# Kernel tuning notes

Hardware: AMD Instinct MI355X
Metric: run time of the kernel (lower is better)

Reference implementation:

```python
import jax, jax.numpy as jnp
import numpy as np

EPS = 1e-7
POS_THR = 0.5   # max_iou assigner positive threshold
NEG_THR = 0.4   # max_iou assigner negative threshold
ALPHA, GAMMA = 0.25, 2.0  # focal loss defaults


def _rand_boxes(key, shape):
    k1, k2 = jax.random.split(key)
    c = jax.random.uniform(k1, shape + (2,), minval=0.05, maxval=0.95)
    wh = jax.random.uniform(k2, shape + (2,), minval=0.02, maxval=0.3)
    return jnp.concatenate([jnp.clip(c - wh / 2, 0, 1), jnp.clip(c + wh / 2, 0, 1)], -1)


def _grid_anchors():
    # 3 anchor sizes per cell on 80x80, 40x40, 20x20 grids -> 25200 anchors, normalized coords
    boxes = []
    for g, sizes in [(80, (0.04, 0.08, 0.12)), (40, (0.1, 0.2, 0.3)), (20, (0.25, 0.45, 0.65))]:
        c = (np.arange(g, dtype=np.float32) + 0.5) / g
        cx, cy = np.meshgrid(c, c)
        for s in sizes:
            boxes.append(np.stack([cx - s / 2, cy - s / 2, cx + s / 2, cy + s / 2], -1).reshape(-1, 4))
    return jnp.asarray(np.concatenate(boxes, 0), dtype=jnp.float32)


def setup_inputs() -> dict:
    key = jax.random.key(0)
    ks = jax.random.split(key, 6)
    N, P, A, C = 32, 100, 25200, 80
    labels = jax.random.randint(ks[0], (N, P), 0, C)
    y_true = jax.nn.one_hot(labels, C, dtype=jnp.float32)
    bbox_true = _rand_boxes(ks[1], (N, P))
    valid = (jnp.arange(P)[None, :] < 30).astype(jnp.float32)  # 30 real boxes, rest zero-padded
    bbox_true = bbox_true * valid[..., None]
    conf_pred = jax.random.uniform(ks[2], (N, A, 1), minval=0.01, maxval=0.99)
    logit_pred = jax.random.uniform(ks[3], (N, A, C), minval=0.01, maxval=0.99)
    bbox_pred = _rand_boxes(ks[4], (N, A))
    anchors = _grid_anchors()
    return {"y_true": y_true, "bbox_true": bbox_true, "conf_pred": conf_pred,
            "logit_pred": logit_pred, "bbox_pred": bbox_pred, "anchors": anchors}


def pairwise_iou(a, b):
    # a: (A,4), b: (P,4) -> (A,P)
    iw = jnp.clip(jnp.minimum(a[:, None, 2], b[None, :, 2]) - jnp.maximum(a[:, None, 0], b[None, :, 0]), 0)
    ih = jnp.clip(jnp.minimum(a[:, None, 3], b[None, :, 3]) - jnp.maximum(a[:, None, 1], b[None, :, 1]), 0)
    inter = iw * ih
    area_a = (a[:, 2] - a[:, 0]) * (a[:, 3] - a[:, 1])
    area_b = (b[:, 2] - b[:, 0]) * (b[:, 3] - b[:, 1])
    return inter / (area_a[:, None] + area_b[None, :] - inter + EPS)


def target_single(y_true, bbox_true, anchors):
    # mask-based equivalent of the dynamic tf.where/gather/scatter target construction
    P = bbox_true.shape[0]
    valid = jnp.any(bbox_true > 0, axis=-1)  # (P,)
    iou = jnp.where(valid[None, :], pairwise_iou(anchors, bbox_true), -1.0)  # (A,P)
    max_iou = iou.max(-1)
    true_idx = iou.argmax(-1)
    pos = max_iou >= POS_THR
    neg = max_iou < NEG_THR
    # low-quality match: best anchor for each valid gt is positive
    gt_max = iou.max(0)
    gt_best = iou.argmax(0)
    lowq = valid & (gt_max > 0)
    pos = pos.astype(jnp.int32).at[gt_best].max(lowq.astype(jnp.int32)).astype(bool)
    true_idx = true_idx.at[gt_best].set(jnp.where(lowq, jnp.arange(P), true_idx[gt_best]))
    neg = neg & ~pos
    state = jnp.where(pos, 1, jnp.where(neg, -1, 0)).astype(jnp.int8)
    C = y_true.shape[-1]
    background = jnp.zeros((C,), jnp.float32).at[0].set(1.0)  # tf.pad(ones,[0,C-1]) default
    tgt_label = jnp.where(pos[:, None], y_true[true_idx], background[None, :])
    tgt_bbox = jnp.where(pos[:, None], bbox_true[true_idx], 0.0)
    return state[:, None], tgt_label, tgt_bbox


def ciou_loss(bt, bp):
    ix1 = jnp.maximum(bt[..., 0], bp[..., 0]); iy1 = jnp.maximum(bt[..., 1], bp[..., 1])
    ix2 = jnp.minimum(bt[..., 2], bp[..., 2]); iy2 = jnp.minimum(bt[..., 3], bp[..., 3])
    inter = jnp.clip(ix2 - ix1, 0) * jnp.clip(iy2 - iy1, 0)
    wt, ht = bt[..., 2] - bt[..., 0], bt[..., 3] - bt[..., 1]
    wp, hp = bp[..., 2] - bp[..., 0], bp[..., 3] - bp[..., 1]
    union = wt * ht + wp * hp - inter + EPS
    iou = inter / union
    cw = jnp.maximum(bt[..., 2], bp[..., 2]) - jnp.minimum(bt[..., 0], bp[..., 0])
    ch = jnp.maximum(bt[..., 3], bp[..., 3]) - jnp.minimum(bt[..., 1], bp[..., 1])
    c2 = cw * cw + ch * ch + EPS
    rho2 = ((bt[..., 0] + bt[..., 2] - bp[..., 0] - bp[..., 2]) ** 2 +
            (bt[..., 1] + bt[..., 3] - bp[..., 1] - bp[..., 3]) ** 2) / 4.0
    v = (4.0 / (np.pi ** 2)) * (jnp.arctan(wt / (ht + EPS)) - jnp.arctan(wp / (hp + EPS))) ** 2
    alpha = jax.lax.stop_gradient(v / (1.0 - iou + v + EPS))
    return 1.0 - iou + rho2 / c2 + alpha * v


def reference(y_true, bbox_true, conf_pred, logit_pred, bbox_pred, anchors):
    state, t_label, t_bbox = jax.vmap(target_single, in_axes=(0, 0, None))(y_true, bbox_true, anchors)
    dtype = logit_pred.dtype
    pw = (state == 1).astype(dtype)   # positive_weight (N,A,1)
    tw = (state != 0).astype(dtype)   # target_weight   (N,A,1)
    avg_factor = jnp.sum(jnp.maximum(jnp.sum(pw, axis=-2), 1.0))
    # score loss: BCE(positive_weight, conf_pred), weighted by target_weight
    p = jnp.clip(conf_pred, EPS, 1.0 - EPS)
    score_l = -(pw * jnp.log(p) + (1.0 - pw) * jnp.log(1.0 - p))
    score_l = jnp.sum(score_l * tw) / avg_factor
    # class loss: focal BCE, weighted by positive_weight
    q = jnp.clip(logit_pred, EPS, 1.0 - EPS)
    pt = t_label * q + (1.0 - t_label) * (1.0 - q)
    at = t_label * ALPHA + (1.0 - t_label) * (1.0 - ALPHA)
    cls_l = -at * (1.0 - pt) ** GAMMA * jnp.log(pt)
    cls_l = jnp.sum(cls_l * pw) / avg_factor
    # bbox loss: CIoU, weighted by positive_weight
    bl = ciou_loss(t_bbox, bbox_pred)[..., None]
    bbox_l = jnp.sum(bl * pw) / avg_factor
    guard = lambda x: jnp.where(jnp.isnan(x) | jnp.isinf(x), jnp.zeros_like(x), x)  # missing_value=0
    return guard(score_l), guard(cls_l), guard(bbox_l)
```

## Files before the change

kernel.cpp:

```cpp
#include <hip/hip_runtime.h>
#include <math.h>

#define EPSF 1e-7f
#define GCHUNK 10
#define NSEG 16

__device__ __forceinline__ int compact_valid(const float4* __restrict__ bt_n, int P, int tid,
                                             float4* scb, int* sidx, float* sarea, int* wcnt) {
    float4 b = make_float4(0.f, 0.f, 0.f, 0.f);
    bool v = false;
    if (tid < P) {
        b = bt_n[tid];
        v = (b.x > 0.f || b.y > 0.f || b.z > 0.f || b.w > 0.f);
    }
    unsigned long long m = __ballot(v);
    int lane = tid & 63, wv = tid >> 6;
    if (lane == 0) wcnt[wv] = __popcll(m);
    int posn = __popcll(m & ((1ull << lane) - 1ull));
    __syncthreads();
    int base = 0;
    for (int w = 0; w < wv; w++) base += wcnt[w];
    int V = wcnt[0] + wcnt[1] + wcnt[2] + wcnt[3];
    if (v) {
        scb[base + posn] = b;
        sidx[base + posn] = tid;
        sarea[base + posn] = (b.z - b.x) * (b.w - b.y);
    }
    __syncthreads();
    return V;
}

__global__ __launch_bounds__(256) void k_gt_all(const float4* __restrict__ bbox_true,
                                                const float4* __restrict__ anchors,
                                                float* __restrict__ pn, float* __restrict__ pd,
                                                int* __restrict__ pi,
                                                unsigned int* __restrict__ done,
                                                int N, int P, int A) {
    __shared__ float4 scb[256];
    __shared__ int    sidx[256];
    __shared__ float  sarea[256];
    __shared__ int    wcnt[4];
    __shared__ float  mn[4][GCHUNK], md[4][GCHUNK];
    __shared__ int    mi[4][GCHUNK];

    int n = blockIdx.y, seg = blockIdx.x, tid = threadIdx.x;
    if (seg == 0 && n == 0 && tid == 0) *done = 0u;
    int lane = tid & 63, wv = tid >> 6;
    int V = compact_valid(bbox_true + (size_t)n * P, P, tid, scb, sidx, sarea, wcnt);
    int len = (A + NSEG - 1) / NSEG;
    int a0 = seg * len;
    int a1 = a0 + len < A ? a0 + len : A;

    for (int c0 = 0; c0 < V; c0 += GCHUNK) {
        int G = V - c0 < GCHUNK ? V - c0 : GCHUNK;
        float bn[GCHUNK], bd[GCHUNK];
        int   bi[GCHUNK];
#pragma unroll
        for (int g = 0; g < GCHUNK; g++) { bn[g] = -1.f; bd[g] = 1.f; bi[g] = 0x7fffffff; }
        for (int a = a0 + tid; a < a1; a += 256) {
            float4 an = anchors[a];
            float aa = (an.z - an.x) * (an.w - an.y);
#pragma unroll
            for (int g = 0; g < GCHUNK; g++) {
                if (g < G) {
                    float4 b = scb[c0 + g];
                    float iw = fminf(an.z, b.z) - fmaxf(an.x, b.x); iw = iw > 0.f ? iw : 0.f;
                    float ih = fminf(an.w, b.w) - fmaxf(an.y, b.y); ih = ih > 0.f ? ih : 0.f;
                    float inter = iw * ih;
                    float den = aa + sarea[c0 + g] - inter + EPSF;
                    if (inter * bd[g] > bn[g] * den) { bn[g] = inter; bd[g] = den; bi[g] = a; }
                }
            }
        }
        for (int off = 32; off > 0; off >>= 1) {
#pragma unroll
            for (int g = 0; g < GCHUNK; g++) {
                float on = __shfl_xor(bn[g], off, 64);
                float od = __shfl_xor(bd[g], off, 64);
                int   oi = __shfl_xor(bi[g], off, 64);
                float l = on * bd[g], r = bn[g] * od;
                if (l > r || (l == r && oi < bi[g])) { bn[g] = on; bd[g] = od; bi[g] = oi; }
            }
        }
        if (lane == 0) {
#pragma unroll
            for (int g = 0; g < GCHUNK; g++) { mn[wv][g] = bn[g]; md[wv][g] = bd[g]; mi[wv][g] = bi[g]; }
        }
        __syncthreads();
        if (tid < G) {
            float Bn = -1.f, Bd = 1.f; int Bi = 0x7fffffff;
            for (int w = 0; w < 4; w++) {
                float cn = mn[w][tid], cd = md[w][tid];
                int ci = mi[w][tid];
                float l = cn * Bd, r = Bn * cd;
                if (l > r || (l == r && ci < Bi)) { Bn = cn; Bd = cd; Bi = ci; }
            }
            int p = sidx[c0 + tid];
            size_t o = ((size_t)n * P + p) * NSEG + seg;
            pn[o] = Bn; pd[o] = Bd; pi[o] = Bi;
        }
        __syncthreads();
    }
}

__global__ __launch_bounds__(128) void k_scatter2(const float4* __restrict__ bbox_true,
                                                  const float* __restrict__ pn,
                                                  const float* __restrict__ pd,
                                                  const int* __restrict__ pi,
                                                  int* __restrict__ ovr_cnt,
                                                  int2* __restrict__ ovr_list,
                                                  int N, int P, int A) {
    int n = blockIdx.x, p = threadIdx.x;
    __shared__ int gb[128];
    __shared__ unsigned char lqs[128];
    __shared__ int cnt;
    if (p == 0) cnt = 0;
    if (p < P) {
        float4 b = bbox_true[(size_t)n * P + p];
        bool valid = (b.x > 0.f || b.y > 0.f || b.z > 0.f || b.w > 0.f);
        int g = 0; bool lq = false;
        if (valid) {
            float Bn = -1.f, Bd = 1.f; int Bi = 0x7fffffff;
            const float* qn = pn + ((size_t)n * P + p) * NSEG;
            const float* qd = pd + ((size_t)n * P + p) * NSEG;
            const int*   qi = pi + ((size_t)n * P + p) * NSEG;
            for (int s = 0; s < NSEG; s++) {
                float cn = qn[s], cd = qd[s]; int ci = qi[s];
                if (cn >= 0.f) {
                    float l = cn * Bd, r = Bn * cd;
                    if (l > r || (l == r && ci < Bi)) { Bn = cn; Bd = cd; Bi = ci; }
                }
            }
            g = Bi;
            lq = (Bn > 0.f);
        }
        gb[p] = g; lqs[p] = lq ? 1 : 0;
    }
    __syncthreads();
    if (p < P) {
        int myidx = gb[p];
        bool anylq = false, islast = true;
        for (int q = 0; q < P; q++) {
            if (gb[q] == myidx) {
                if (lqs[q]) anylq = true;
                if (q > p) islast = false;
            }
        }
        if (islast && anylq) {
            int s = atomicAdd(&cnt, 1);
            ovr_list[(size_t)n * P + s] = make_int2(myidx, lqs[p] ? p : -2);
        }
    }
    __syncthreads();
    if (p == 0) ovr_cnt[n] = cnt;
}

__global__ __launch_bounds__(256) void k_fused(const float4* __restrict__ bbox_true,
                                               const float4* __restrict__ anchors,
                                               const float* __restrict__ conf,
                                               const float* __restrict__ logit,
                                               const float4* __restrict__ bbox_pred,
                                               const float* __restrict__ y_true,
                                               const int* __restrict__ ovr_cnt,
                                               const int2* __restrict__ ovr_list,
                                               double* __restrict__ partial,
                                               unsigned int* __restrict__ done,
                                               float* __restrict__ out,
                                               int N, int P, int A, int C, int BX) {
    int tid = threadIdx.x;
    int n = blockIdx.y;
    int a = blockIdx.x * blockDim.x + tid;
    int lane = tid & 63, wv = tid >> 6;

    __shared__ float4 scb[256];
    __shared__ int    sidx[256];
    __shared__ float  sarea[256];
    __shared__ int    wcnt[4];
    __shared__ int    sflag[256];
    __shared__ int    plist[256];
    __shared__ int    pw4[4];

    sflag[tid] = -1;
    int V = compact_valid(bbox_true + (size_t)n * P, P, tid, scb, sidx, sarea, wcnt);
    int cnt = ovr_cnt[n];
    if (tid < cnt) {
        int2 e = ovr_list[(size_t)n * P + tid];
        int local = e.x - blockIdx.x * 256;
        if (local >= 0 && local < 256) sflag[local] = e.y;
    }
    __syncthreads();

    double sc = 0.0, cl = 0.0, bb = 0.0, pc = 0.0;
    bool pos = false;
    int t = 0;
    if (a < A) {
        float4 an = anchors[a];
        float aa = (an.z - an.x) * (an.w - an.y);
        float bn = -1.f, bd = 1.f; int bi = 0;
        for (int k = 0; k < V; k++) {
            float4 b = scb[k];
            float iw = fminf(an.z, b.z) - fmaxf(an.x, b.x); iw = iw > 0.f ? iw : 0.f;
            float ih = fminf(an.w, b.w) - fmaxf(an.y, b.y); ih = ih > 0.f ? ih : 0.f;
            float inter = iw * ih;
            float den = aa + sarea[k] - inter + EPSF;
            if (inter * bd > bn * den) { bn = inter; bd = den; bi = sidx[k]; }
        }
        bool neg;
        if (V > 0) { pos = (bn >= 0.5f * bd); neg = (bn < 0.4f * bd); }
        else       { pos = false; neg = true; }
        int ov = sflag[tid];
        pos = pos || (ov != -1);
        neg = neg && !pos;
        t = (ov >= 0) ? ov : bi;

        size_t o = (size_t)n * A + a;
        float p = conf[o];
        p = fminf(fmaxf(p, EPSF), 1.f - EPSF);
        if (pos || neg) sc = (double)(-logf(pos ? p : 1.f - p));
        if (pos) {
            pc = 1.0;
            float4 bt = bbox_true[(size_t)n * P + t];
            float4 bp = bbox_pred[o];
            float ix1 = fmaxf(bt.x, bp.x), iy1 = fmaxf(bt.y, bp.y);
            float ix2 = fminf(bt.z, bp.z), iy2 = fminf(bt.w, bp.w);
            float iw = ix2 - ix1; iw = iw > 0.f ? iw : 0.f;
            float ih = iy2 - iy1; ih = ih > 0.f ? ih : 0.f;
            float inter = iw * ih;
            float wt = bt.z - bt.x, ht = bt.w - bt.y;
            float wp = bp.z - bp.x, hp = bp.w - bp.y;
            float uni = wt * ht + wp * hp - inter + EPSF;
            float iou = inter / uni;
            float cw = fmaxf(bt.z, bp.z) - fminf(bt.x, bp.x);
            float ch = fmaxf(bt.w, bp.w) - fminf(bt.y, bp.y);
            float c2 = cw * cw + ch * ch + EPSF;
            float dx = bt.x + bt.z - bp.x - bp.z;
            float dy = bt.y + bt.w - bp.y - bp.w;
            float rho2 = (dx * dx + dy * dy) * 0.25f;
            float dd = atanf(wt / (ht + EPSF)) - atanf(wp / (hp + EPSF));
            float vv = 0.40528473456935109f * dd * dd;
            float al = vv / (1.f - iou + vv + EPSF);
            bb = (double)(1.f - iou + rho2 / c2 + al * vv);
        }
    }

    {
        unsigned long long m = __ballot(pos);
        if (lane == 0) pw4[wv] = __popcll(m);
        int posn = __popcll(m & ((1ull << lane) - 1ull));
        __syncthreads();
        int base = 0;
        for (int w = 0; w < wv; w++) base += pw4[w];
        int npos = pw4[0] + pw4[1] + pw4[2] + pw4[3];
        if (pos) plist[base + posn] = tid | (t << 8);
        __syncthreads();

        for (int i = wv; i < npos; i += 4) {
            int e = plist[i];
            int la = e & 255, tt = e >> 8;
            size_t o = (size_t)n * A + (size_t)blockIdx.x * 256 + la;
            const float* lg = logit + o * C;
            const float* yt = y_true + ((size_t)n * P + tt) * C;
            float s = 0.f;
            for (int c = lane; c < C; c += 64) {
                float tl = yt[c];
                float q = fminf(fmaxf(lg[c], EPSF), 1.f - EPSF);
                float pt = tl * q + (1.f - tl) * (1.f - q);
                float at = tl * 0.25f + (1.f - tl) * 0.75f;
                float om = 1.f - pt;
                s += -at * om * om * logf(pt);
            }
            for (int off = 32; off > 0; off >>= 1) s += __shfl_down(s, off, 64);
            if (lane == 0) cl += (double)s;
        }
    }

    for (int off = 32; off > 0; off >>= 1) {
        sc += __shfl_down(sc, off, 64);
        cl += __shfl_down(cl, off, 64);
        bb += __shfl_down(bb, off, 64);
        pc += __shfl_down(pc, off, 64);
    }
    __shared__ double sred[4][4];
    if (lane == 0) { sred[wv][0] = sc; sred[wv][1] = cl; sred[wv][2] = bb; sred[wv][3] = pc; }
    __syncthreads();
    __shared__ int amLast;
    if (tid == 0) {
        double r0 = 0, r1 = 0, r2 = 0, r3 = 0;
        for (int w = 0; w < 4; w++) {
            r0 += sred[w][0]; r1 += sred[w][1]; r2 += sred[w][2]; r3 += sred[w][3];
        }
        double* row = partial + ((size_t)n * BX + blockIdx.x) * 4;
        row[0] = r0; row[1] = r1; row[2] = r2; row[3] = r3;
        __threadfence();
        unsigned int old = atomicAdd(done, 1u);
        amLast = (old == (unsigned int)(N * BX) - 1u) ? 1 : 0;
    }
    __syncthreads();
    if (!amLast) return;
    __threadfence();

    __shared__ double sh[256];
    __shared__ double res[3];
    __shared__ double shn[64];
    double s0 = 0, s1 = 0, s2 = 0;
    int total = N * BX;
    for (int i = tid; i < total; i += 256) {
        const double* r = partial + (size_t)i * 4;
        s0 += r[0]; s1 += r[1]; s2 += r[2];
    }
    double vals[3] = {s0, s1, s2};
    for (int k = 0; k < 3; k++) {
        sh[tid] = vals[k];
        __syncthreads();
        for (int s = 128; s > 0; s >>= 1) {
            if (tid < s) sh[tid] += sh[tid + s];
            __syncthreads();
        }
        if (tid == 0) res[k] = sh[0];
        __syncthreads();
    }
    int chunks = 256 / N;
    double pcs = 0;
    int nn = tid / chunks, cc = tid % chunks;
    if (nn < N) {
        int per = (BX + chunks - 1) / chunks;
        int j0 = cc * per, j1 = (j0 + per < BX) ? j0 + per : BX;
        for (int j = j0; j < j1; j++) pcs += partial[((size_t)nn * BX + j) * 4 + 3];
    }
    sh[tid] = pcs;
    __syncthreads();
    if (tid < N) {
        double s = 0;
        for (int c2 = 0; c2 < chunks; c2++) s += sh[tid * chunks + c2];
        shn[tid] = s > 1.0 ? s : 1.0;
    }
    __syncthreads();
    if (tid == 0) {
        double avg = 0;
        for (int i = 0; i < N; i++) avg += shn[i];
        for (int k = 0; k < 3; k++) {
            double x = res[k] / avg;
            if (isnan(x) || isinf(x)) x = 0.0;
            out[k] = (float)x;
        }
    }
}

extern "C" void kernel_launch(void* const* d_in, const int* in_sizes, int n_in,
                              void* d_out, int out_size, void* d_ws, size_t ws_size,
                              hipStream_t stream) {
    const float* y_true    = (const float*)d_in[0];
    const float* bbox_true = (const float*)d_in[1];
    const float* conf      = (const float*)d_in[2];
    const float* logit     = (const float*)d_in[3];
    const float* bboxp     = (const float*)d_in[4];
    const float* anchors   = (const float*)d_in[5];

    int A = in_sizes[5] / 4;
    int N = in_sizes[2] / A;
    int P = in_sizes[1] / (4 * N);
    int C = in_sizes[0] / (N * P);

    int BX = (A + 255) / 256;

    char* w = (char*)d_ws;
    auto alloc = [&](size_t bytes) -> void* {
        void* r = (void*)w;
        w += (bytes + 15) & ~(size_t)15;
        return r;
    };
    float*  pn      = (float*)alloc(sizeof(float) * (size_t)N * P * NSEG);
    float*  pd      = (float*)alloc(sizeof(float) * (size_t)N * P * NSEG);
    int*    pi      = (int*)alloc(sizeof(int) * (size_t)N * P * NSEG);
    int*    ovr_cnt = (int*)alloc(sizeof(int) * (size_t)N);
    int2*   ovr_list= (int2*)alloc(sizeof(int2) * (size_t)N * P);
    double* partial = (double*)alloc(sizeof(double) * (size_t)N * BX * 4);
    unsigned int* done = (unsigned int*)alloc(sizeof(unsigned int));

    dim3 gS(NSEG, N);
    k_gt_all<<<gS, 256, 0, stream>>>((const float4*)bbox_true, (const float4*)anchors,
                                     pn, pd, pi, done, N, P, A);

    k_scatter2<<<N, 128, 0, stream>>>((const float4*)bbox_true, pn, pd, pi,
                                      ovr_cnt, ovr_list, N, P, A);

    dim3 gA(BX, N);
    k_fused<<<gA, 256, 0, stream>>>((const float4*)bbox_true, (const float4*)anchors,
                                    conf, logit, (const float4*)bboxp, y_true,
                                    ovr_cnt, ovr_list, partial, done, (float*)d_out,
                                    N, P, A, C, BX);
}
```

Before: 500.0 us.

## Prefetch per-anchor loads early, reuse shared GT boxes, split final reduction kernel

Per-anchor inputs (conf, anchor, predicted box, override list entry) are now loaded at kernel entry, before the shared-memory compaction barrier, so their latency overlaps the setup. The matched ground-truth box is taken from shared memory (tracked best box or an inverse index map) instead of a second global load. The last-block atomic counter with threadfences is replaced by a separate single-block finalize kernel. This costs one extra launch in exchange for removing the atomic and the fences, and adds a little register and shared-memory pressure.

```diff
diff --git a/kernel.cpp b/kernel.cpp
--- a/kernel.cpp
+++ b/kernel.cpp
@@ -6,7 +6,8 @@
 #define NSEG 16
 
 __device__ __forceinline__ int compact_valid(const float4* __restrict__ bt_n, int P, int tid,
-                                             float4* scb, int* sidx, float* sarea, int* wcnt) {
+                                             float4* scb, int* sidx, float* sarea,
+                                             int* sinv, int* wcnt) {
     float4 b = make_float4(0.f, 0.f, 0.f, 0.f);
     bool v = false;
     if (tid < P) {
@@ -25,6 +26,7 @@
         scb[base + posn] = b;
         sidx[base + posn] = tid;
         sarea[base + posn] = (b.z - b.x) * (b.w - b.y);
+        if (sinv) sinv[tid] = base + posn;
     }
     __syncthreads();
     return V;
@@ -34,7 +36,6 @@
                                                 const float4* __restrict__ anchors,
                                                 float* __restrict__ pn, float* __restrict__ pd,
                                                 int* __restrict__ pi,
-                                                unsigned int* __restrict__ done,
                                                 int N, int P, int A) {
     __shared__ float4 scb[256];
     __shared__ int    sidx[256];
@@ -44,9 +45,8 @@
     __shared__ int    mi[4][GCHUNK];
 
     int n = blockIdx.y, seg = blockIdx.x, tid = threadIdx.x;
-    if (seg == 0 && n == 0 && tid == 0) *done = 0u;
     int lane = tid & 63, wv = tid >> 6;
-    int V = compact_valid(bbox_true + (size_t)n * P, P, tid, scb, sidx, sarea, wcnt);
+    int V = compact_valid(bbox_true + (size_t)n * P, P, tid, scb, sidx, sarea, nullptr, wcnt);
     int len = (A + NSEG - 1) / NSEG;
     int a0 = seg * len;
     int a1 = a0 + len < A ? a0 + len : A;
@@ -164,8 +164,6 @@
                                                const int* __restrict__ ovr_cnt,
                                                const int2* __restrict__ ovr_list,
                                                double* __restrict__ partial,
-                                               unsigned int* __restrict__ done,
-                                               float* __restrict__ out,
                                                int N, int P, int A, int C, int BX) {
     int tid = threadIdx.x;
     int n = blockIdx.y;
@@ -175,18 +173,25 @@
     __shared__ float4 scb[256];
     __shared__ int    sidx[256];
     __shared__ float  sarea[256];
+    __shared__ int    sinv[256];
     __shared__ int    wcnt[4];
     __shared__ int    sflag[256];
     __shared__ int    plist[256];
     __shared__ int    pw4[4];
 
+    size_t o = (size_t)n * A + (size_t)(a < A ? a : A - 1);
+    float  pconf = conf[o];
+    float4 anch  = anchors[a < A ? a : A - 1];
+    float4 bp    = bbox_pred[o];
+    int    cnt   = ovr_cnt[n];
+    int2   epre  = make_int2(0, 0);
+    if (tid < P) epre = ovr_list[(size_t)n * P + tid];
+
     sflag[tid] = -1;
-    int V = compact_valid(bbox_true + (size_t)n * P, P, tid, scb, sidx, sarea, wcnt);
-    int cnt = ovr_cnt[n];
+    int V = compact_valid(bbox_true + (size_t)n * P, P, tid, scb, sidx, sarea, sinv, wcnt);
     if (tid < cnt) {
-        int2 e = ovr_list[(size_t)n * P + tid];
-        int local = e.x - blockIdx.x * 256;
-        if (local >= 0 && local < 256) sflag[local] = e.y;
+        int local = epre.x - blockIdx.x * 256;
+        if (local >= 0 && local < 256) sflag[local] = epre.y;
     }
     __syncthreads();
 
@@ -194,16 +199,16 @@
     bool pos = false;
     int t = 0;
     if (a < A) {
-        float4 an = anchors[a];
-        float aa = (an.z - an.x) * (an.w - an.y);
+        float aa = (anch.z - anch.x) * (anch.w - anch.y);
         float bn = -1.f, bd = 1.f; int bi = 0;
+        float4 bbest = make_float4(0.f, 0.f, 0.f, 0.f);
         for (int k = 0; k < V; k++) {
             float4 b = scb[k];
-            float iw = fminf(an.z, b.z) - fmaxf(an.x, b.x); iw = iw > 0.f ? iw : 0.f;
-            float ih = fminf(an.w, b.w) - fmaxf(an.y, b.y); ih = ih > 0.f ? ih : 0.f;
+            float iw = fminf(anch.z, b.z) - fmaxf(anch.x, b.x); iw = iw > 0.f ? iw : 0.f;
+            float ih = fminf(anch.w, b.w) - fmaxf(anch.y, b.y); ih = ih > 0.f ? ih : 0.f;
             float inter = iw * ih;
             float den = aa + sarea[k] - inter + EPSF;
-            if (inter * bd > bn * den) { bn = inter; bd = den; bi = sidx[k]; }
+            if (inter * bd > bn * den) { bn = inter; bd = den; bi = sidx[k]; bbest = b; }
         }
         bool neg;
         if (V > 0) { pos = (bn >= 0.5f * bd); neg = (bn < 0.4f * bd); }
@@ -213,14 +218,11 @@
         neg = neg && !pos;
         t = (ov >= 0) ? ov : bi;
 
-        size_t o = (size_t)n * A + a;
-        float p = conf[o];
-        p = fminf(fmaxf(p, EPSF), 1.f - EPSF);
+        float p = fminf(fmaxf(pconf, EPSF), 1.f - EPSF);
         if (pos || neg) sc = (double)(-logf(pos ? p : 1.f - p));
         if (pos) {
             pc = 1.0;
-            float4 bt = bbox_true[(size_t)n * P + t];
-            float4 bp = bbox_pred[o];
+            float4 bt = (ov >= 0) ? scb[sinv[ov]] : bbest;
             float ix1 = fmaxf(bt.x, bp.x), iy1 = fmaxf(bt.y, bp.y);
             float ix2 = fminf(bt.z, bp.z), iy2 = fminf(bt.w, bp.w);
             float iw = ix2 - ix1; iw = iw > 0.f ? iw : 0.f;
@@ -257,8 +259,8 @@
         for (int i = wv; i < npos; i += 4) {
             int e = plist[i];
             int la = e & 255, tt = e >> 8;
-            size_t o = (size_t)n * A + (size_t)blockIdx.x * 256 + la;
-            const float* lg = logit + o * C;
+            size_t oo = (size_t)n * A + (size_t)blockIdx.x * 256 + la;
+            const float* lg = logit + oo * C;
             const float* yt = y_true + ((size_t)n * P + tt) * C;
             float s = 0.f;
             for (int c = lane; c < C; c += 64) {
@@ -283,7 +285,6 @@
     __shared__ double sred[4][4];
     if (lane == 0) { sred[wv][0] = sc; sred[wv][1] = cl; sred[wv][2] = bb; sred[wv][3] = pc; }
     __syncthreads();
-    __shared__ int amLast;
     if (tid == 0) {
         double r0 = 0, r1 = 0, r2 = 0, r3 = 0;
         for (int w = 0; w < 4; w++) {
@@ -291,20 +292,20 @@
         }
         double* row = partial + ((size_t)n * BX + blockIdx.x) * 4;
         row[0] = r0; row[1] = r1; row[2] = r2; row[3] = r3;
-        __threadfence();
-        unsigned int old = atomicAdd(done, 1u);
-        amLast = (old == (unsigned int)(N * BX) - 1u) ? 1 : 0;
-    }
-    __syncthreads();
-    if (!amLast) return;
-    __threadfence();
-
-    __shared__ double sh[256];
+    }
+}
+
+__global__ __launch_bounds__(256) void k_final(const double* __restrict__ partial,
+                                               float* __restrict__ out, int N, int BX) {
+    const int FT = 256;
+    int tid = threadIdx.x;
+    __shared__ double sh[FT];
     __shared__ double res[3];
     __shared__ double shn[64];
+
     double s0 = 0, s1 = 0, s2 = 0;
     int total = N * BX;
-    for (int i = tid; i < total; i += 256) {
+    for (int i = tid; i < total; i += FT) {
         const double* r = partial + (size_t)i * 4;
         s0 += r[0]; s1 += r[1]; s2 += r[2];
     }
@@ -319,13 +320,13 @@
         if (tid == 0) res[k] = sh[0];
         __syncthreads();
     }
-    int chunks = 256 / N;
+    int chunks = FT / N;
     double pcs = 0;
-    int nn = tid / chunks, cc = tid % chunks;
-    if (nn < N) {
+    int n = tid / chunks, c = tid % chunks;
+    if (n < N) {
         int per = (BX + chunks - 1) / chunks;
-        int j0 = cc * per, j1 = (j0 + per < BX) ? j0 + per : BX;
-        for (int j = j0; j < j1; j++) pcs += partial[((size_t)nn * BX + j) * 4 + 3];
+        int j0 = c * per, j1 = (j0 + per < BX) ? j0 + per : BX;
+        for (int j = j0; j < j1; j++) pcs += partial[((size_t)n * BX + j) * 4 + 3];
     }
     sh[tid] = pcs;
     __syncthreads();
@@ -375,11 +376,10 @@
     int*    ovr_cnt = (int*)alloc(sizeof(int) * (size_t)N);
     int2*   ovr_list= (int2*)alloc(sizeof(int2) * (size_t)N * P);
     double* partial = (double*)alloc(sizeof(double) * (size_t)N * BX * 4);
-    unsigned int* done = (unsigned int*)alloc(sizeof(unsigned int));
 
     dim3 gS(NSEG, N);
     k_gt_all<<<gS, 256, 0, stream>>>((const float4*)bbox_true, (const float4*)anchors,
-                                     pn, pd, pi, done, N, P, A);
+                                     pn, pd, pi, N, P, A);
 
     k_scatter2<<<N, 128, 0, stream>>>((const float4*)bbox_true, pn, pd, pi,
                                       ovr_cnt, ovr_list, N, P, A);
@@ -387,6 +387,7 @@
     dim3 gA(BX, N);
     k_fused<<<gA, 256, 0, stream>>>((const float4*)bbox_true, (const float4*)anchors,
                                     conf, logit, (const float4*)bboxp, y_true,
-                                    ovr_cnt, ovr_list, partial, done, (float*)d_out,
-                                    N, P, A, C, BX);
-}
+                                    ovr_cnt, ovr_list, partial, N, P, A, C, BX);
+
+    k_final<<<1, 256, 0, stream>>>(partial, (float*)d_out, N, BX);
+}
```

New measurement: 426.3 us. -14.7%, faster.
